# Performance work log

Hardware: AMD Instinct MI355X
Metric: run time of the kernel (lower is better)

## Reference

```python
import jax, jax.numpy as jnp
import numpy as np

B, T, C, N = 4, 4, 32, 16384
F_OUT = 64
K = 9          # kernel_size
DIL = 1        # dilation
PAD = 4 * DIL  # padding * dilation, as in the torch module


def _unfold1d(a, k, pad, dil):
    """im2col along the last axis. a: [..., N] -> [..., k, N] (stride 1)."""
    ap = jnp.pad(a, [(0, 0)] * (a.ndim - 1) + [(pad, pad)])
    n = a.shape[-1]
    idx = jnp.arange(k)[:, None] * dil + jnp.arange(n)[None, :]  # [k, N]
    return ap[..., idx]


def setup_inputs() -> dict:
    key = jax.random.key(0)
    k1, k2, k3 = jax.random.split(key, 3)
    x = jax.random.normal(k1, (B, T, C, N), dtype=jnp.float32)
    coords = jax.random.normal(k2, (B, T, 3, N), dtype=jnp.float32)
    weight = jax.random.normal(k3, (T, F_OUT, C, K), dtype=jnp.float32) * 0.05
    return {"x": x, "coords": coords, "weight": weight, "sigma": 2}


def reference(x, coords, weight, sigma):
    # im2col windows of features: [B, T, C, K, N]  (channel-major then kernel,
    # matching F.unfold's (C*K, L) layout)
    win = _unfold1d(x, K, PAD, DIL)
    # im2col windows of coords: [B, T, 3, K, N]
    cw = _unfold1d(coords, K, PAD, DIL)
    # subtract center tap (k = K//2)
    diff = cw - cw[:, :, :, K // 2, :][:, :, :, None, :]
    d2 = jnp.sum(diff * diff, axis=2)  # [B, T, K, N]
    # safe sqrt: forward-identical, avoids NaN grads at the zero-distance center
    d = jnp.where(d2 > 0, jnp.sqrt(jnp.where(d2 > 0, d2, 1.0)), 0.0)
    # distance weights, clamped at 0 (torch: dist_weights[dist_weights<0]=0)
    w = jnp.maximum(1.0 - d / sigma, 0.0)  # [B, T, K, N]
    # weight windows; repeat over C in torch == broadcast over C here
    win = win * w[:, :, None, :, :]  # [B, T, C, K, N]
    # batched matmul over flattened (C*K): out[b,t,f,n]
    out = jnp.einsum('btckn,tfck->btfn', win, weight)
    return out
```

## Files before the change

### kernel.cpp

```cpp
#include <hip/hip_runtime.h>
#include <math.h>

#define Bd   4
#define Td   4
#define Cd   32
#define Nd   16384
#define Fd   64
#define Kd   9
#define PADd 4
#define NT   128
#define NROWS (NT + 2*PADd)
#define NCHUNK (NROWS/4)
#define XPITCH 140
#define EPIT 36

typedef __attribute__((ext_vector_type(8))) short  short8;
typedef __attribute__((ext_vector_type(4))) float  float4v;

#define A_WS_BYTES ((size_t)Td * Kd * 4 * 64 * 8 * 2)

#define SM_XSN 0
#define SM_WL  8960
#define SM_CS  13568
#define SM_BYTES 18432

__device__ __forceinline__ float sigma_as_float(const void* p) {
    int iv = *(const int*)p;
    if (iv > 0 && iv < 1000000) return (float)iv;
    return __int_as_float(iv);
}

__device__ __forceinline__ unsigned short f32_to_bf16_rne(float v) {
    unsigned int a = __float_as_uint(v);
    a += 0x7fffu + ((a >> 16) & 1u);
    return (unsigned short)(a >> 16);
}

__global__ void prep_weights(const float* __restrict__ w, unsigned short* __restrict__ a) {
    int idx = blockIdx.x * 256 + threadIdx.x;
    if (idx >= Td * Kd * 4 * 64 * 8) return;
    int j    = idx & 7;
    int lane = (idx >> 3) & 63;
    int ft   = (idx >> 9) & 3;
    int k    = (idx >> 11) % Kd;
    int t    = idx / (Kd * 4 * 64 * 8);
    int m = lane & 15, q = lane >> 4;
    int f = ft * 16 + m;
    int c = q * 8 + j;
    float v = w[(((size_t)t * Fd + f) * Cd + c) * Kd + k];
    a[idx] = f32_to_bf16_rne(v);
}

__global__ __launch_bounds__(256, 4)
void swconv_mfma3(const float* __restrict__ x,
                  const float* __restrict__ coords,
                  const unsigned short* __restrict__ aw,
                  const void* __restrict__ sigma_p,
                  float* __restrict__ out)
{
    __shared__ __align__(16) unsigned char smem[SM_BYTES];
    unsigned short (*xsn)[XPITCH] = (unsigned short (*)[XPITCH])(smem + SM_XSN);
    float (*wl)[NT]               = (float (*)[NT])(smem + SM_WL);
    float (*cs)[NROWS]            = (float (*)[NROWS])(smem + SM_CS);

    const int tid  = threadIdx.x;
    const int lane = tid & 63;
    const int wv   = tid >> 6;
    const int tile = blockIdx.x, t = blockIdx.y, b = blockIdx.z;
    const int n0   = tile * NT;
    const float inv_sigma = 1.0f / sigma_as_float(sigma_p);

    const float* xbt = x + (size_t)(b * Td + t) * Cd * Nd;
    #pragma unroll 2
    for (int i = tid; i < Cd * NCHUNK; i += 256) {
        int c  = i / NCHUNK;
        int rq = i - c * NCHUNK;
        int nf = n0 - PADd + rq * 4;
        float4 v = make_float4(0.f, 0.f, 0.f, 0.f);
        if (nf >= 0 && nf < Nd)
            v = *reinterpret_cast<const float4*>(xbt + (size_t)c * Nd + nf);
        ushort4 u;
        u.x = f32_to_bf16_rne(v.x);
        u.y = f32_to_bf16_rne(v.y);
        u.z = f32_to_bf16_rne(v.z);
        u.w = f32_to_bf16_rne(v.w);
        *reinterpret_cast<ushort4*>(&xsn[c][rq * 4]) = u;
    }

    const float* cbt = coords + (size_t)(b * Td + t) * 3 * Nd;
    for (int i = tid; i < 3 * NROWS; i += 256) {
        int c = i / NROWS, r = i - c * NROWS;
        int n = n0 - PADd + r;
        cs[c][r] = (n >= 0 && n < Nd) ? cbt[(size_t)c * Nd + n] : 0.0f;
    }

    const int m = lane & 15, q = lane >> 4;
    const unsigned short* Abase = aw + (size_t)t * Kd * 4 * 64 * 8 + (size_t)lane * 8;
    short8 afr[2][4];
    #pragma unroll
    for (int ft = 0; ft < 4; ++ft)
        afr[0][ft] = *reinterpret_cast<const short8*>(Abase + (size_t)ft * 512);

    __syncthreads();

    {
        int nl   = wv * 32 + (lane & 31);
        int half = lane >> 5;
        int il   = nl + PADd;
        float c0 = cs[0][il], c1 = cs[1][il], c2 = cs[2][il];
        int k0 = half ? 5 : 0, k1 = half ? Kd : 5;
        #pragma unroll
        for (int k = k0; k < k1; ++k) {
            float d0 = cs[0][nl + k] - c0;
            float d1 = cs[1][nl + k] - c1;
            float d2 = cs[2][nl + k] - c2;
            float s = d0 * d0 + d1 * d1 + d2 * d2;
            float d = (s > 0.0f) ? sqrtf(s) : 0.0f;
            wl[k][nl] = fmaxf(1.0f - d * inv_sigma, 0.0f);
        }
    }

    float4v acc[4][2];
    #pragma unroll
    for (int ft = 0; ft < 4; ++ft)
        #pragma unroll
        for (int nt = 0; nt < 2; ++nt)
            acc[ft][nt] = (float4v){0.f, 0.f, 0.f, 0.f};
    const float4v zero4 = {0.f, 0.f, 0.f, 0.f};

    for (int k = 0; k < Kd; ++k) {
        const int cur = k & 1;
        if (k + 1 < Kd) {
            #pragma unroll
            for (int ft = 0; ft < 4; ++ft)
                afr[cur ^ 1][ft] = *reinterpret_cast<const short8*>(Abase + (size_t)((k + 1) * 4 + ft) * 512);
        }
        #pragma unroll
        for (int nt = 0; nt < 2; ++nt) {
            const int ncol = wv * 32 + nt * 16 + m;
            const int r    = ncol + k;
            const unsigned short* bp = &xsn[q * 8][r];
            unsigned int p0 = (unsigned int)bp[0]          | ((unsigned int)bp[XPITCH]     << 16);
            unsigned int p1 = (unsigned int)bp[2 * XPITCH] | ((unsigned int)bp[3 * XPITCH] << 16);
            unsigned int p2 = (unsigned int)bp[4 * XPITCH] | ((unsigned int)bp[5 * XPITCH] << 16);
            unsigned int p3 = (unsigned int)bp[6 * XPITCH] | ((unsigned int)bp[7 * XPITCH] << 16);
            uint4 pk = {p0, p1, p2, p3};
            short8 bfr = *reinterpret_cast<short8*>(&pk);
            const float wgt = wl[k][ncol];
            #pragma unroll
            for (int ft = 0; ft < 4; ++ft) {
                float4v d = __builtin_amdgcn_mfma_f32_16x16x32_bf16(afr[cur][ft], bfr, zero4, 0, 0, 0);
                acc[ft][nt][0] = fmaf(wgt, d[0], acc[ft][nt][0]);
                acc[ft][nt][1] = fmaf(wgt, d[1], acc[ft][nt][1]);
                acc[ft][nt][2] = fmaf(wgt, d[2], acc[ft][nt][2]);
                acc[ft][nt][3] = fmaf(wgt, d[3], acc[ft][nt][3]);
            }
        }
    }

    __syncthreads();
    float (*epi)[EPIT] = (float (*)[EPIT])(smem + (size_t)wv * 32 * EPIT * 4);

    float* ob = out + (size_t)(b * Td + t) * Fd * Nd + n0 + wv * 32;
    #pragma unroll
    for (int fc = 0; fc < 2; ++fc) {
        #pragma unroll
        for (int ft2 = 0; ft2 < 2; ++ft2) {
            const int ft = fc * 2 + ft2;
            #pragma unroll
            for (int nt = 0; nt < 2; ++nt) {
                const int np = nt * 16 + m;
                #pragma unroll
                for (int rr = 0; rr < 4; ++rr)
                    epi[ft2 * 16 + q * 4 + rr][np] = acc[ft][nt][rr];
            }
        }
        #pragma unroll
        for (int inst = 0; inst < 4; ++inst) {
            const int fl = inst * 8 + (lane >> 3);
            const int np = (lane & 7) * 4;
            float4 v = *reinterpret_cast<const float4*>(&epi[fl][np]);
            *reinterpret_cast<float4*>(ob + (size_t)(fc * 32 + fl) * Nd + np) = v;
        }
    }
}

__global__ __launch_bounds__(256, 4)
void swconv_f32_kernel(const float* __restrict__ x,
                       const float* __restrict__ coords,
                       const float* __restrict__ weight,
                       const void*  __restrict__ sigma_p,
                       float* __restrict__ out)
{
    __shared__ float xsf[Cd][NROWS + 1];
    __shared__ float csf[3][NROWS + 1];
    const int tid = threadIdx.x;
    const int tile = blockIdx.x, t = blockIdx.y, b = blockIdx.z;
    const int n0 = tile * NT;
    const float inv_sigma = 1.0f / sigma_as_float(sigma_p);

    const float* xbt = x + (size_t)(b * Td + t) * Cd * Nd;
    for (int idx = tid; idx < Cd * NROWS; idx += 256) {
        int c = idx / NROWS, i = idx - c * NROWS, n = n0 - PADd + i;
        xsf[c][i] = (n >= 0 && n < Nd) ? xbt[(size_t)c * Nd + n] : 0.0f;
    }
    const float* cbt = coords + (size_t)(b * Td + t) * 3 * Nd;
    for (int idx = tid; idx < 3 * NROWS; idx += 256) {
        int c = idx / NROWS, i = idx - c * NROWS, n = n0 - PADd + i;
        csf[c][i] = (n >= 0 && n < Nd) ? cbt[(size_t)c * Nd + n] : 0.0f;
    }
    __syncthreads();
    if (tid >= NT) return;

    float wk[Kd];
    {
        const float c0 = csf[0][tid + PADd], c1 = csf[1][tid + PADd], c2 = csf[2][tid + PADd];
        #pragma unroll
        for (int k = 0; k < Kd; ++k) {
            float d0 = csf[0][tid + k] - c0, d1 = csf[1][tid + k] - c1, d2 = csf[2][tid + k] - c2;
            float s = d0 * d0 + d1 * d1 + d2 * d2;
            float d = (s > 0.0f) ? sqrtf(s) : 0.0f;
            wk[k] = fmaxf(1.0f - d * inv_sigma, 0.0f);
        }
    }
    float accf[Fd];
    #pragma unroll
    for (int f = 0; f < Fd; ++f) accf[f] = 0.0f;
    const float* wt = weight + (size_t)t * Fd * Cd * Kd;
    for (int c = 0; c < Cd; ++c) {
        float xv[Kd];
        #pragma unroll
        for (int k = 0; k < Kd; ++k) xv[k] = xsf[c][tid + k];
        const float* wp = wt + c * Kd;
        #pragma unroll
        for (int k = 0; k < Kd; ++k) {
            float v = xv[k] * wk[k];
            #pragma unroll
            for (int f = 0; f < Fd; ++f)
                accf[f] = fmaf(v, wp[(size_t)f * Cd * Kd + k], accf[f]);
        }
    }
    float* op = out + (size_t)(b * Td + t) * Fd * Nd + n0 + tid;
    #pragma unroll
    for (int f = 0; f < Fd; ++f) op[(size_t)f * Nd] = accf[f];
}

extern "C" void kernel_launch(void* const* d_in, const int* in_sizes, int n_in,
                              void* d_out, int out_size, void* d_ws, size_t ws_size,
                              hipStream_t stream) {
    const float* x      = (const float*)d_in[0];
    const float* coords = (const float*)d_in[1];
    const float* weight = (const float*)d_in[2];
    const void*  sigma  = d_in[3];
    float* out = (float*)d_out;

    if (ws_size >= A_WS_BYTES) {
        unsigned short* aw = (unsigned short*)d_ws;
        prep_weights<<<(Td * Kd * 4 * 64 * 8 + 255) / 256, 256, 0, stream>>>(weight, aw);
        dim3 grid(Nd / NT, Td, Bd);
        swconv_mfma3<<<grid, dim3(256), 0, stream>>>(x, coords, aw, sigma, out);
    } else {
        dim3 grid(Nd / NT, Td, Bd);
        swconv_f32_kernel<<<grid, dim3(256), 0, stream>>>(x, coords, weight, sigma, out);
    }
}
```

Before: 130.0 us.

## Fold distance weight into fp16 B operand and accumulate inside MFMA

```diff
diff --git a/kernel.cpp b/kernel.cpp
--- a/kernel.cpp
+++ b/kernel.cpp
@@ -11,18 +11,20 @@
 #define NT   128
 #define NROWS (NT + 2*PADd)
 #define NCHUNK (NROWS/4)
-#define XPITCH 140
-#define EPIT 36
-
-typedef __attribute__((ext_vector_type(8))) short  short8;
-typedef __attribute__((ext_vector_type(4))) float  float4v;
+#define XP    40
+#define EPIT  36
+
+typedef __attribute__((ext_vector_type(8))) _Float16 half8;
+typedef __attribute__((ext_vector_type(4))) float    float4v;
 
 #define A_WS_BYTES ((size_t)Td * Kd * 4 * 64 * 8 * 2)
 
-#define SM_XSN 0
-#define SM_WL  8960
-#define SM_CS  13568
+#define SM_XT  0
+#define SM_WL  10880
+#define SM_CS  15488
 #define SM_BYTES 18432
+
+union FragU { uint4 u; half8 h; };
 
 __device__ __forceinline__ float sigma_as_float(const void* p) {
     int iv = *(const int*)p;
@@ -30,10 +32,9 @@
     return __int_as_float(iv);
 }
 
-__device__ __forceinline__ unsigned short f32_to_bf16_rne(float v) {
-    unsigned int a = __float_as_uint(v);
-    a += 0x7fffu + ((a >> 16) & 1u);
-    return (unsigned short)(a >> 16);
+__device__ __forceinline__ unsigned short f32_to_f16_bits(float f) {
+    _Float16 h = (_Float16)f;
+    return *reinterpret_cast<unsigned short*>(&h);
 }
 
 __global__ void prep_weights(const float* __restrict__ w, unsigned short* __restrict__ a) {
@@ -48,20 +49,20 @@
     int f = ft * 16 + m;
     int c = q * 8 + j;
     float v = w[(((size_t)t * Fd + f) * Cd + c) * Kd + k];
-    a[idx] = f32_to_bf16_rne(v);
+    a[idx] = f32_to_f16_bits(v);
 }
 
 __global__ __launch_bounds__(256, 4)
-void swconv_mfma3(const float* __restrict__ x,
+void swconv_mfma4(const float* __restrict__ x,
                   const float* __restrict__ coords,
                   const unsigned short* __restrict__ aw,
                   const void* __restrict__ sigma_p,
                   float* __restrict__ out)
 {
     __shared__ __align__(16) unsigned char smem[SM_BYTES];
-    unsigned short (*xsn)[XPITCH] = (unsigned short (*)[XPITCH])(smem + SM_XSN);
-    float (*wl)[NT]               = (float (*)[NT])(smem + SM_WL);
-    float (*cs)[NROWS]            = (float (*)[NROWS])(smem + SM_CS);
+    unsigned short (*xt)[XP] = (unsigned short (*)[XP])(smem + SM_XT);
+    unsigned int (*wlp)[NT]  = (unsigned int (*)[NT])(smem + SM_WL);
+    float (*cs)[NROWS]       = (float (*)[NROWS])(smem + SM_CS);
 
     const int tid  = threadIdx.x;
     const int lane = tid & 63;
@@ -79,12 +80,11 @@
         float4 v = make_float4(0.f, 0.f, 0.f, 0.f);
         if (nf >= 0 && nf < Nd)
             v = *reinterpret_cast<const float4*>(xbt + (size_t)c * Nd + nf);
-        ushort4 u;
-        u.x = f32_to_bf16_rne(v.x);
-        u.y = f32_to_bf16_rne(v.y);
-        u.z = f32_to_bf16_rne(v.z);
-        u.w = f32_to_bf16_rne(v.w);
-        *reinterpret_cast<ushort4*>(&xsn[c][rq * 4]) = u;
+        int r = rq * 4;
+        xt[r + 0][c] = f32_to_f16_bits(v.x);
+        xt[r + 1][c] = f32_to_f16_bits(v.y);
+        xt[r + 2][c] = f32_to_f16_bits(v.z);
+        xt[r + 3][c] = f32_to_f16_bits(v.w);
     }
 
     const float* cbt = coords + (size_t)(b * Td + t) * 3 * Nd;
@@ -96,10 +96,10 @@
 
     const int m = lane & 15, q = lane >> 4;
     const unsigned short* Abase = aw + (size_t)t * Kd * 4 * 64 * 8 + (size_t)lane * 8;
-    short8 afr[2][4];
+    FragU afr[2][4];
     #pragma unroll
     for (int ft = 0; ft < 4; ++ft)
-        afr[0][ft] = *reinterpret_cast<const short8*>(Abase + (size_t)ft * 512);
+        afr[0][ft].u = *reinterpret_cast<const uint4*>(Abase + (size_t)ft * 512);
 
     __syncthreads();
 
@@ -116,7 +116,8 @@
             float d2 = cs[2][nl + k] - c2;
             float s = d0 * d0 + d1 * d1 + d2 * d2;
             float d = (s > 0.0f) ? sqrtf(s) : 0.0f;
-            wl[k][nl] = fmaxf(1.0f - d * inv_sigma, 0.0f);
+            float w = fmaxf(1.0f - d * inv_sigma, 0.0f);
+            wlp[k][nl] = (unsigned int)f32_to_f16_bits(w) * 0x00010001u;
         }
     }
 
@@ -126,35 +127,25 @@
         #pragma unroll
         for (int nt = 0; nt < 2; ++nt)
             acc[ft][nt] = (float4v){0.f, 0.f, 0.f, 0.f};
-    const float4v zero4 = {0.f, 0.f, 0.f, 0.f};
 
     for (int k = 0; k < Kd; ++k) {
         const int cur = k & 1;
         if (k + 1 < Kd) {
             #pragma unroll
             for (int ft = 0; ft < 4; ++ft)
-                afr[cur ^ 1][ft] = *reinterpret_cast<const short8*>(Abase + (size_t)((k + 1) * 4 + ft) * 512);
+                afr[cur ^ 1][ft].u = *reinterpret_cast<const uint4*>(Abase + (size_t)((k + 1) * 4 + ft) * 512);
         }
         #pragma unroll
         for (int nt = 0; nt < 2; ++nt) {
             const int ncol = wv * 32 + nt * 16 + m;
             const int r    = ncol + k;
-            const unsigned short* bp = &xsn[q * 8][r];
-            unsigned int p0 = (unsigned int)bp[0]          | ((unsigned int)bp[XPITCH]     << 16);
-            unsigned int p1 = (unsigned int)bp[2 * XPITCH] | ((unsigned int)bp[3 * XPITCH] << 16);
-            unsigned int p2 = (unsigned int)bp[4 * XPITCH] | ((unsigned int)bp[5 * XPITCH] << 16);
-            unsigned int p3 = (unsigned int)bp[6 * XPITCH] | ((unsigned int)bp[7 * XPITCH] << 16);
-            uint4 pk = {p0, p1, p2, p3};
-            short8 bfr = *reinterpret_cast<short8*>(&pk);
-            const float wgt = wl[k][ncol];
-            #pragma unroll
-            for (int ft = 0; ft < 4; ++ft) {
-                float4v d = __builtin_amdgcn_mfma_f32_16x16x32_bf16(afr[cur][ft], bfr, zero4, 0, 0, 0);
-                acc[ft][nt][0] = fmaf(wgt, d[0], acc[ft][nt][0]);
-                acc[ft][nt][1] = fmaf(wgt, d[1], acc[ft][nt][1]);
-                acc[ft][nt][2] = fmaf(wgt, d[2], acc[ft][nt][2]);
-                acc[ft][nt][3] = fmaf(wgt, d[3], acc[ft][nt][3]);
-            }
+            FragU xv; xv.u = *reinterpret_cast<const uint4*>(&xt[r][q * 8]);
+            unsigned int wp = wlp[k][ncol];
+            FragU ww; ww.u = make_uint4(wp, wp, wp, wp);
+            half8 bfr = xv.h * ww.h;
+            #pragma unroll
+            for (int ft = 0; ft < 4; ++ft)
+                acc[ft][nt] = __builtin_amdgcn_mfma_f32_16x16x32_f16(afr[cur][ft].h, bfr, acc[ft][nt], 0, 0, 0);
         }
     }
 
@@ -258,7 +249,7 @@
         unsigned short* aw = (unsigned short*)d_ws;
         prep_weights<<<(Td * Kd * 4 * 64 * 8 + 255) / 256, 256, 0, stream>>>(weight, aw);
         dim3 grid(Nd / NT, Td, Bd);
-        swconv_mfma3<<<grid, dim3(256), 0, stream>>>(x, coords, aw, sigma, out);
+        swconv_mfma4<<<grid, dim3(256), 0, stream>>>(x, coords, aw, sigma, out);
     } else {
         dim3 grid(Nd / NT, Td, Bd);
         swconv_f32_kernel<<<grid, dim3(256), 0, stream>>>(x, coords, weight, sigma, out);
```

Result: faster. 111.3 us (-14.3%).
